# Kernel optimization log

Hardware: AMD Instinct MI355X
Metric: run time of the kernel (lower is better)

Reference implementation:

```python
import jax, jax.numpy as jnp
import numpy as np

N = 50000      # nodes
E = 800000     # edges (avg degree 16)
F_IN = 128     # input feature dim
HID = 64       # hidden_channels
HEADS = 4
OUT = 64       # out_channels


def _gatv2_layer(x, src, dst, Wl, Wr, att, bias, heads, ch, n):
    # lin_l (source) and lin_r (target) projections -> [N, H, C]
    xl = (x @ Wl).reshape(n, heads, ch)
    xr = (x @ Wr).reshape(n, heads, ch)
    # per-edge GATv2 attention logits: a^T LeakyReLU(xl_j + xr_i)
    e = jax.nn.leaky_relu(xl[src] + xr[dst], negative_slope=0.2)  # [E, H, C]
    score = jnp.einsum('ehc,hc->eh', e, att)                      # [E, H]
    # segment softmax over incoming edges of each destination node
    m = jax.ops.segment_max(score, dst, num_segments=n)           # [N, H]
    m = jnp.where(jnp.isfinite(m), m, 0.0)
    p = jnp.exp(score - m[dst])
    denom = jax.ops.segment_sum(p, dst, num_segments=n)           # [N, H]
    alpha = p / (denom[dst] + 1e-16)                              # [E, H]
    # weighted scatter-aggregate of source messages xl_j
    out = jax.ops.segment_sum(alpha[..., None] * xl[src], dst, num_segments=n)
    return out.reshape(n, heads * ch) + bias


def setup_inputs() -> dict:
    key = jax.random.key(0)
    ks = jax.random.split(key, 16)

    def w(k, shape, fan_in):
        return (jax.random.normal(k, shape, dtype=jnp.float32) / np.sqrt(fan_in)).astype(jnp.float32)

    return {
        'x': jax.random.normal(ks[0], (N, F_IN), dtype=jnp.float32),
        'Wl1': w(ks[1], (F_IN, HEADS * HID), F_IN),
        'Wr1': w(ks[2], (F_IN, HEADS * HID), F_IN),
        'att1': w(ks[3], (HEADS, HID), HID),
        'b1': jnp.zeros((HEADS * HID,), jnp.float32),
        'Wl2': w(ks[4], (HEADS * HID, HEADS * HID), HEADS * HID),
        'Wr2': w(ks[5], (HEADS * HID, HEADS * HID), HEADS * HID),
        'att2': w(ks[6], (HEADS, HID), HID),
        'b2': jnp.zeros((HEADS * HID,), jnp.float32),
        'Wl3': w(ks[7], (HEADS * HID, OUT), HEADS * HID),
        'Wr3': w(ks[8], (HEADS * HID, OUT), HEADS * HID),
        'att3': w(ks[9], (1, OUT), OUT),
        'b3': jnp.zeros((OUT,), jnp.float32),
        'Wlin': w(ks[10], (OUT, HID), OUT),
        'blin': jnp.zeros((HID,), jnp.float32),
        'edge_index': jax.random.randint(ks[11], (2, E), 0, N, dtype=jnp.int64
                                         if jax.config.read('jax_enable_x64') else jnp.int32),
    }


def reference(x, Wl1, Wr1, att1, b1, Wl2, Wr2, att2, b2, Wl3, Wr3, att3, b3, Wlin, blin, edge_index):
    src, dst = edge_index[0], edge_index[1]
    h = jax.nn.elu(_gatv2_layer(x, src, dst, Wl1, Wr1, att1, b1, HEADS, HID, N))
    h = jax.nn.elu(_gatv2_layer(h, src, dst, Wl2, Wr2, att2, b2, HEADS, HID, N))
    h = _gatv2_layer(h, src, dst, Wl3, Wr3, att3, b3, 1, OUT, N)
    # F.dropout(p=0.5, training=False) -> identity in eval mode
    return h @ Wlin + blin
```

## Files before the change

kernel.cpp:

```cpp
#include <hip/hip_runtime.h>
#include <hip/hip_fp16.h>

#define NN 50000
#define EE 800000

typedef float f32x4 __attribute__((ext_vector_type(4)));
typedef _Float16 f16x8 __attribute__((ext_vector_type(8)));
typedef _Float16 f16x4 __attribute__((ext_vector_type(4)));
typedef _Float16 f16x2 __attribute__((ext_vector_type(2)));

__global__ void hist_kernel(const int* __restrict__ dst, int* __restrict__ counts, int E) {
    int idx = blockIdx.x * blockDim.x + threadIdx.x;
    int stride = gridDim.x * blockDim.x;
    for (int e = idx; e < E; e += stride)
        atomicAdd(&counts[dst[e]], 1);
}

__global__ void scan_phaseA(const int* __restrict__ counts, int* __restrict__ bsum, int n) {
    __shared__ int buf[256];
    int b = blockIdx.x, t = threadIdx.x;
    int i = b * 256 + t;
    buf[t] = (i < n) ? counts[i] : 0;
    __syncthreads();
#pragma unroll
    for (int off = 128; off; off >>= 1) {
        if (t < off) buf[t] += buf[t + off];
        __syncthreads();
    }
    if (t == 0) bsum[b] = buf[0];
}

__global__ void scan_phaseB(int* __restrict__ bsum, int* __restrict__ row_off_n, int nb) {
    __shared__ int buf[256];
    int t = threadIdx.x;
    int v = (t < nb) ? bsum[t] : 0;
    buf[t] = v;
    __syncthreads();
#pragma unroll
    for (int off = 1; off < 256; off <<= 1) {
        int x = (t >= off) ? buf[t - off] : 0;
        __syncthreads();
        buf[t] += x;
        __syncthreads();
    }
    if (t < nb) bsum[t] = buf[t] - v;
    if (t == 255) *row_off_n = buf[255];
}

__global__ void scan_phaseC(const int* __restrict__ counts, const int* __restrict__ bsum,
                            int* __restrict__ row_off, int n) {
    __shared__ int buf[256];
    int b = blockIdx.x, t = threadIdx.x;
    int i = b * 256 + t;
    int v = (i < n) ? counts[i] : 0;
    buf[t] = v;
    __syncthreads();
#pragma unroll
    for (int off = 1; off < 256; off <<= 1) {
        int x = (t >= off) ? buf[t - off] : 0;
        __syncthreads();
        buf[t] += x;
        __syncthreads();
    }
    if (i < n) row_off[i] = bsum[b] + buf[t] - v;
}

__global__ void scatter_kernel(const int* __restrict__ src, const int* __restrict__ dst,
                               const int* __restrict__ row_off, int* __restrict__ cursor,
                               int* __restrict__ esrc, int E) {
    int idx = blockIdx.x * blockDim.x + threadIdx.x;
    int stride = gridDim.x * blockDim.x;
    for (int e = idx; e < E; e += stride) {
        int d = dst[e];
        int pos = row_off[d] + atomicAdd(&cursor[d], 1);
        esrc[pos] = src[e];
    }
}

__device__ __forceinline__ void wfrag_store(__half* o, int K, int col, int k, float v) {
    int KS = K >> 5;
    int cgni = col >> 4, l15 = col & 15;
    int ks = k >> 5, qq = (k >> 3) & 3, ee = k & 7;
    size_t flat = ((size_t)(cgni * KS + ks) * 64 + qq * 16 + l15) * 8 + ee;
    o[flat] = __float2half_rn(v);
}

__global__ void prep_all(const float* __restrict__ Wl1, const float* __restrict__ Wr1,
                         const float* __restrict__ Wl2, const float* __restrict__ Wr2,
                         const float* __restrict__ Wl3, const float* __restrict__ Wr3,
                         const float* __restrict__ Wlin,
                         __half* __restrict__ w1, __half* __restrict__ w2,
                         __half* __restrict__ w3, __half* __restrict__ w4,
                         const float* __restrict__ x, __half* __restrict__ xf, int n4x) {
    int idx = blockIdx.x * blockDim.x + threadIdx.x;
    if (idx < 233472) {
        const float* W; __half* o; int K, Nc, roff, li;
        if (idx < 65536) {
            K = 128; Nc = 256; o = w1;
            if (idx < 32768) { W = Wl1; li = idx; roff = 0; }
            else             { W = Wr1; li = idx - 32768; roff = 256; }
        } else if (idx < 196608) {
            K = 256; Nc = 256; o = w2;
            if (idx < 131072) { W = Wl2; li = idx - 65536; roff = 0; }
            else              { W = Wr2; li = idx - 131072; roff = 256; }
        } else if (idx < 229376) {
            K = 256; Nc = 64; o = w3;
            if (idx < 212992) { W = Wl3; li = idx - 196608; roff = 0; }
            else              { W = Wr3; li = idx - 212992; roff = 64; }
        } else {
            K = 64; Nc = 64; o = w4; W = Wlin; li = idx - 229376; roff = 0;
        }
        int k = li / Nc, n = li - k * Nc;
        wfrag_store(o, K, roff + n, k, W[li]);
    } else {
        int xi = idx - 233472;
        if (xi < n4x) {
            float4 v = *(const float4*)(x + (size_t)xi * 4);
            f16x4 h = {(_Float16)v.x, (_Float16)v.y, (_Float16)v.z, (_Float16)v.w};
            *(f16x4*)((_Float16*)xf + (size_t)xi * 4) = h;
        }
    }
}

template <int KS, int COLG>
__global__ __launch_bounds__(COLG * 256) void gemm_ws(
        const __half* __restrict__ A, const __half* __restrict__ Bt,
        int M, int nTiles, int Nc, int splitCol,
        __half* __restrict__ outL, __half* __restrict__ outR,
        float* __restrict__ outF, const float* __restrict__ bias) {
    constexpr int K = KS * 32;
    int tid = threadIdx.x;
    int lane = tid & 63;
    int w = tid >> 6;
    int rs = w & 3;
    int cg = w >> 2;
    int l15 = lane & 15, q = lane >> 4;
    int colbase = blockIdx.y * (COLG * 64) + cg * 64;

    const _Float16* Ap = (const _Float16*)A;
    const f16x8* Bf = (const f16x8*)Bt;
    int cgni0 = (blockIdx.y * COLG + cg) * 4;

    f16x8 bfrag[KS][4];
#pragma unroll
    for (int ks = 0; ks < KS; ++ks)
#pragma unroll
        for (int ni = 0; ni < 4; ++ni)
            bfrag[ks][ni] = Bf[((size_t)(cgni0 + ni) * KS + ks) * 64 + lane];

    int tile = blockIdx.x;
    if (tile >= nTiles) return;

    f16x8 afrag[KS];
    {
        int row = tile * 64 + rs * 16 + l15;
        if (row >= M) row = M - 1;
        const _Float16* ap = Ap + (size_t)row * K + q * 8;
#pragma unroll
        for (int ks = 0; ks < KS; ++ks) afrag[ks] = *(const f16x8*)(ap + ks * 32);
    }

    while (true) {
        int next = tile + gridDim.x;
        bool has = (next < nTiles);
        f16x8 anext[KS];
        if (has) {
            int row = next * 64 + rs * 16 + l15;
            if (row >= M) row = M - 1;
            const _Float16* ap = Ap + (size_t)row * K + q * 8;
#pragma unroll
            for (int ks = 0; ks < KS; ++ks) anext[ks] = *(const f16x8*)(ap + ks * 32);
        }

        f32x4 acc[4] = {};
#pragma unroll
        for (int ks = 0; ks < KS; ++ks)
#pragma unroll
            for (int ni = 0; ni < 4; ++ni)
                acc[ni] = __builtin_amdgcn_mfma_f32_16x16x32_f16(afrag[ks], bfrag[ks][ni], acc[ni], 0, 0, 0);

#pragma unroll
        for (int ni = 0; ni < 4; ++ni) {
            int gc = colbase + ni * 16 + l15;
            if (outF) {
                float bv = bias ? bias[gc] : 0.f;
#pragma unroll
                for (int r = 0; r < 4; ++r) {
                    int gr = tile * 64 + rs * 16 + q * 4 + r;
                    if (gr < M) outF[(size_t)gr * Nc + gc] = acc[ni][r] + bv;
                }
            } else {
                __half* dp = outL; int cc = gc;
                if (gc >= splitCol) { dp = outR; cc = gc - splitCol; }
#pragma unroll
                for (int r = 0; r < 4; ++r) {
                    int gr = tile * 64 + rs * 16 + q * 4 + r;
                    if (gr < M) dp[(size_t)gr * splitCol + cc] = __float2half_rn(acc[ni][r]);
                }
            }
        }
        if (!has) break;
#pragma unroll
        for (int ks = 0; ks < KS; ++ks) afrag[ks] = anext[ks];
        tile = next;
    }
}

template <int CTRL>
__device__ __forceinline__ float dpp_add_f32(float x) {
    int y = __builtin_amdgcn_mov_dpp(__float_as_int(x), CTRL, 0xF, 0xF, true);
    return x + __int_as_float(y);
}

__global__ __launch_bounds__(256, 8) void gat_gather_h4(
        const __half* __restrict__ xl, const __half* __restrict__ xr,
        const float* __restrict__ att, const float* __restrict__ bias,
        const int* __restrict__ row_off, const int* __restrict__ esrc,
        __half* __restrict__ out, int n) {
    const float LOG2E = 1.44269504f;
    int wave = threadIdx.x >> 6;
    int lane = threadIdx.x & 63;
    int node = blockIdx.x * 4 + wave;
    if (node >= n) return;
    int slot = lane >> 5;
    unsigned jj = lane & 31;

    const uint4* xl16 = (const uint4*)xl;

    f16x2 xrv[4];
    *(uint4*)(&xrv[0]) = ((const uint4*)xr)[((unsigned)node << 5) + jj];

    float4 a0 = *(const float4*)(att + jj * 8);
    float4 a1 = *(const float4*)(att + jj * 8 + 4);
    f16x2 atv[4] = {
        {(_Float16)(a0.x * LOG2E), (_Float16)(a0.y * LOG2E)},
        {(_Float16)(a0.z * LOG2E), (_Float16)(a0.w * LOG2E)},
        {(_Float16)(a1.x * LOG2E), (_Float16)(a1.y * LOG2E)},
        {(_Float16)(a1.z * LOG2E), (_Float16)(a1.w * LOG2E)}};
    const f16x2 k02 = {(_Float16)0.2f, (_Float16)0.2f};

    float acc[8] = {};
    float L = 0.f;

    int e0 = row_off[node], e1 = row_off[node + 1];
    int elast = (e1 > e0) ? e1 - 1 : 0;

    int sA = esrc[min(e0 + 0 + slot, elast)];
    int sB = esrc[min(e0 + 2 + slot, elast)];
    int sC = esrc[min(e0 + 4 + slot, elast)];
    int sD = esrc[min(e0 + 6 + slot, elast)];
    uint4 A = xl16[((unsigned)sA << 5) + jj];
    uint4 B = xl16[((unsigned)sB << 5) + jj];
    uint4 C = xl16[((unsigned)sC << 5) + jj];
    uint4 D = xl16[((unsigned)sD << 5) + jj];

#define H4_PHASE(BUF, EB)                                                     \
    {                                                                         \
        f16x2 v[4];                                                           \
        *(uint4*)(&v[0]) = BUF;                                               \
        float t = 0.f;                                                        \
        _Pragma("unroll")                                                     \
        for (int k = 0; k < 4; ++k) {                                         \
            f16x2 s = v[k] + xrv[k];                                          \
            f16x2 r = __builtin_elementwise_max(s, s * k02);                  \
            t = __builtin_amdgcn_fdot2(r, atv[k], t, false);                  \
        }                                                                     \
        t = dpp_add_f32<0xB1>(t);                                             \
        t = dpp_add_f32<0x4E>(t);                                             \
        t = dpp_add_f32<0x141>(t);                                            \
        float p = exp2f(t);                                                   \
        p = ((EB) + slot < e1) ? p : 0.f;                                     \
        L += p;                                                               \
        _Pragma("unroll")                                                     \
        for (int k = 0; k < 4; ++k) {                                         \
            acc[2 * k]     = fmaf((float)v[k].x, p, acc[2 * k]);              \
            acc[2 * k + 1] = fmaf((float)v[k].y, p, acc[2 * k + 1]);          \
        }                                                                     \
    }

    {
        int e = e0;
        while (true) {
            int ns = esrc[min(e + 8 + slot, elast)];
            H4_PHASE(A, e)
            A = xl16[((unsigned)ns << 5) + jj];
            e += 2; if (e >= e1) break;
            ns = esrc[min(e + 8 + slot, elast)];
            H4_PHASE(B, e)
            B = xl16[((unsigned)ns << 5) + jj];
            e += 2; if (e >= e1) break;
            ns = esrc[min(e + 8 + slot, elast)];
            H4_PHASE(C, e)
            C = xl16[((unsigned)ns << 5) + jj];
            e += 2; if (e >= e1) break;
            ns = esrc[min(e + 8 + slot, elast)];
            H4_PHASE(D, e)
            D = xl16[((unsigned)ns << 5) + jj];
            e += 2; if (e >= e1) break;
        }
    }
#undef H4_PHASE

#pragma unroll
    for (int k = 0; k < 8; ++k) acc[k] += __shfl_xor(acc[k], 32);
    L += __shfl_xor(L, 32);

    if (slot == 0) {
        float inv = 1.f / (L + 1e-16f);
        float4 b0 = *(const float4*)(bias + jj * 8);
        float4 b1v = *(const float4*)(bias + jj * 8 + 4);
        float bb[8] = {b0.x, b0.y, b0.z, b0.w, b1v.x, b1v.y, b1v.z, b1v.w};
        f16x8 o0;
#pragma unroll
        for (int k = 0; k < 8; ++k) {
            float vA = acc[k] * inv + bb[k];
            vA = vA > 0.f ? vA : __expf(vA) - 1.f;
            o0[k] = (_Float16)vA;
        }
        *(f16x8*)((_Float16*)out + ((size_t)node << 8) + jj * 8) = o0;
    }
}

__global__ __launch_bounds__(256, 8) void gat_gather_h1(
        const __half* __restrict__ xl, const __half* __restrict__ xr,
        const float* __restrict__ att, const float* __restrict__ bias,
        const int* __restrict__ row_off, const int* __restrict__ esrc,
        __half* __restrict__ out, int n) {
    const float LOG2E = 1.44269504f;
    int wave = threadIdx.x >> 6;
    int lane = threadIdx.x & 63;
    int node = blockIdx.x * 4 + wave;
    if (node >= n) return;
    int eslot = lane >> 3;
    unsigned j = lane & 7;

    const uint4* xl16 = (const uint4*)xl;

    f16x2 xrv[4];
    *(uint4*)(&xrv[0]) = ((const uint4*)xr)[((unsigned)node << 3) + j];

    float4 a0 = *(const float4*)(att + j * 8);
    float4 a1 = *(const float4*)(att + j * 8 + 4);
    f16x2 atv[4] = {
        {(_Float16)(a0.x * LOG2E), (_Float16)(a0.y * LOG2E)},
        {(_Float16)(a0.z * LOG2E), (_Float16)(a0.w * LOG2E)},
        {(_Float16)(a1.x * LOG2E), (_Float16)(a1.y * LOG2E)},
        {(_Float16)(a1.z * LOG2E), (_Float16)(a1.w * LOG2E)}};
    const f16x2 k02 = {(_Float16)0.2f, (_Float16)0.2f};

    float acc[8] = {};
    float L = 0.f;

    int e0 = row_off[node], e1 = row_off[node + 1];
    int elast = (e1 > e0) ? e1 - 1 : 0;

    int sA = esrc[min(e0 +  0 + eslot, elast)];
    int sB = esrc[min(e0 +  8 + eslot, elast)];
    int sC = esrc[min(e0 + 16 + eslot, elast)];
    uint4 A = xl16[((unsigned)sA << 3) + j];
    uint4 B = xl16[((unsigned)sB << 3) + j];
    uint4 C = xl16[((unsigned)sC << 3) + j];

#define H1_PHASE(R, EB)                                                       \
    {                                                                         \
        f16x2 v[4];                                                           \
        *(uint4*)(&v[0]) = R;                                                 \
        float t0 = 0.f, t1 = 0.f;                                             \
        {                                                                     \
            f16x2 s0 = v[0] + xrv[0];                                         \
            f16x2 r0 = __builtin_elementwise_max(s0, s0 * k02);               \
            t0 = __builtin_amdgcn_fdot2(r0, atv[0], t0, false);               \
            f16x2 s1 = v[1] + xrv[1];                                         \
            f16x2 r1 = __builtin_elementwise_max(s1, s1 * k02);               \
            t0 = __builtin_amdgcn_fdot2(r1, atv[1], t0, false);               \
            f16x2 s2 = v[2] + xrv[2];                                         \
            f16x2 r2 = __builtin_elementwise_max(s2, s2 * k02);               \
            t1 = __builtin_amdgcn_fdot2(r2, atv[2], t1, false);               \
            f16x2 s3 = v[3] + xrv[3];                                         \
            f16x2 r3 = __builtin_elementwise_max(s3, s3 * k02);               \
            t1 = __builtin_amdgcn_fdot2(r3, atv[3], t1, false);               \
        }                                                                     \
        float t = t0 + t1;                                                    \
        t = dpp_add_f32<0xB1>(t);                                             \
        t = dpp_add_f32<0x4E>(t);                                             \
        t = dpp_add_f32<0x141>(t);                                            \
        float p = exp2f(t);                                                   \
        p = ((EB) + eslot < e1) ? p : 0.f;                                    \
        L += p;                                                               \
        _Pragma("unroll")                                                     \
        for (int k = 0; k < 4; ++k) {                                         \
            acc[2 * k]     = fmaf((float)v[k].x, p, acc[2 * k]);              \
            acc[2 * k + 1] = fmaf((float)v[k].y, p, acc[2 * k + 1]);          \
        }                                                                     \
    }

    {
        int e = e0;
        while (true) {
            int ns = esrc[min(e + 24 + eslot, elast)];
            H1_PHASE(A, e)
            A = xl16[((unsigned)ns << 3) + j];
            e += 8; if (e >= e1) break;
            ns = esrc[min(e + 24 + eslot, elast)];
            H1_PHASE(B, e)
            B = xl16[((unsigned)ns << 3) + j];
            e += 8; if (e >= e1) break;
            ns = esrc[min(e + 24 + eslot, elast)];
            H1_PHASE(C, e)
            C = xl16[((unsigned)ns << 3) + j];
            e += 8; if (e >= e1) break;
        }
    }
#undef H1_PHASE

#pragma unroll
    for (int k = 0; k < 8; ++k) {
        acc[k] += __shfl_xor(acc[k], 8);
        acc[k] += __shfl_xor(acc[k], 16);
        acc[k] += __shfl_xor(acc[k], 32);
    }
    L += __shfl_xor(L, 8);
    L += __shfl_xor(L, 16);
    L += __shfl_xor(L, 32);

    if (eslot == 0) {
        float inv = 1.f / (L + 1e-16f);
        float4 b0 = *(const float4*)(bias + j * 8);
        float4 b1v = *(const float4*)(bias + j * 8 + 4);
        float bb[8] = {b0.x, b0.y, b0.z, b0.w, b1v.x, b1v.y, b1v.z, b1v.w};
        f16x8 ov;
#pragma unroll
        for (int k = 0; k < 8; ++k)
            ov[k] = (_Float16)(acc[k] * inv + bb[k]);
        *(f16x8*)((_Float16*)out + ((size_t)node << 6) + j * 8) = ov;
    }
}

extern "C" void kernel_launch(void* const* d_in, const int* in_sizes, int n_in,
                              void* d_out, int out_size, void* d_ws, size_t ws_size,
                              hipStream_t stream) {
    const float* x    = (const float*)d_in[0];
    const float* Wl1  = (const float*)d_in[1];
    const float* Wr1  = (const float*)d_in[2];
    const float* att1 = (const float*)d_in[3];
    const float* b1   = (const float*)d_in[4];
    const float* Wl2  = (const float*)d_in[5];
    const float* Wr2  = (const float*)d_in[6];
    const float* att2 = (const float*)d_in[7];
    const float* b2   = (const float*)d_in[8];
    const float* Wl3  = (const float*)d_in[9];
    const float* Wr3  = (const float*)d_in[10];
    const float* att3 = (const float*)d_in[11];
    const float* b3   = (const float*)d_in[12];
    const float* Wlin = (const float*)d_in[13];
    const float* blin = (const float*)d_in[14];
    const int*   ei   = (const int*)d_in[15];
    const int* src = ei;
    const int* dst = ei + EE;

    const int N = NN, E = EE;
    const int NB = (N + 255) / 256;

    __half* xf = (__half*)d_ws;
    __half* xl = xf + (size_t)N * 128;
    __half* xr = xl + (size_t)N * 256;
    __half* H  = xr + (size_t)N * 256;
    __half* G  = H + (size_t)N * 256;
    __half* w1 = G + (size_t)N * 64;
    __half* w2 = w1 + 65536;
    __half* w3 = w2 + 131072;
    __half* w4 = w3 + 32768;
    int* row_off = (int*)(w4 + 4096);
    int* tmp     = row_off + (N + 1);
    int* esrc    = tmp + 2 * N;
    int* bsum    = esrc + E;

    hipMemsetAsync(tmp, 0, (size_t)2 * N * sizeof(int), stream);
    hist_kernel<<<1024, 256, 0, stream>>>(dst, tmp, E);
    scan_phaseA<<<NB, 256, 0, stream>>>(tmp, bsum, N);
    scan_phaseB<<<1, 256, 0, stream>>>(bsum, row_off + N, NB);
    scan_phaseC<<<NB, 256, 0, stream>>>(tmp, bsum, row_off, N);
    scatter_kernel<<<1024, 256, 0, stream>>>(src, dst, row_off, tmp + N, esrc, E);

    int n4x = N * 128 / 4;
    prep_all<<<(233472 + n4x + 255) / 256, 256, 0, stream>>>(
        Wl1, Wr1, Wl2, Wr2, Wl3, Wr3, Wlin, w1, w2, w3, w4, x, xf, n4x);

    int nTiles = (N + 63) / 64;
    int gatherBlocks = (N + 3) / 4;

    gemm_ws<4, 2><<<dim3(128, 4), 512, 0, stream>>>(
        xf, w1, N, nTiles, 512, 256, xl, xr, nullptr, nullptr);
    gat_gather_h4<<<gatherBlocks, 256, 0, stream>>>(xl, xr, att1, b1, row_off, esrc, H, N);

    gemm_ws<8, 2><<<dim3(128, 4), 512, 0, stream>>>(
        H, w2, N, nTiles, 512, 256, xl, xr, nullptr, nullptr);
    gat_gather_h4<<<gatherBlocks, 256, 0, stream>>>(xl, xr, att2, b2, row_off, esrc, H, N);

    gemm_ws<8, 2><<<dim3(256, 1), 512, 0, stream>>>(
        H, w3, N, nTiles, 128, 64, xl, xr, nullptr, nullptr);
    gat_gather_h1<<<gatherBlocks, 256, 0, stream>>>(xl, xr, att3, b3, row_off, esrc, G, N);

    gemm_ws<2, 1><<<dim3(512, 1), 256, 0, stream>>>(
        G, w4, N, nTiles, 64, 64, nullptr, nullptr, (float*)d_out, blin);
}
```

Measured before the change: 463.1 us.

## Swizzle GEMM block order, shrink gather blocks, use raw v_exp_f32

Flattens the 2D GEMM grid into a 1D launch and remaps block IDs so that groups of 8 row tiles across all 4 column groups run next to each other. The intent is to improve L2 reuse of the A rows. The gather kernels now run 2 waves per block instead of 4, giving finer scheduling granularity for the irregular per-node edge counts. exp2f is replaced by inline-asm v_exp_f32, which skips the range and denormal handling; this could misbehave on extreme inputs and adds an s_nop.

```diff
diff --git a/kernel.cpp b/kernel.cpp
--- a/kernel.cpp
+++ b/kernel.cpp
@@ -122,7 +122,7 @@
     }
 }
 
-template <int KS, int COLG>
+template <int KS, int COLG, int NBX>
 __global__ __launch_bounds__(COLG * 256) void gemm_ws(
         const __half* __restrict__ A, const __half* __restrict__ Bt,
         int M, int nTiles, int Nc, int splitCol,
@@ -135,11 +135,22 @@
     int rs = w & 3;
     int cg = w >> 2;
     int l15 = lane & 15, q = lane >> 4;
-    int colbase = blockIdx.y * (COLG * 64) + cg * 64;
+
+    int bx, by;
+    if constexpr (NBX > 0) {
+        int bid = blockIdx.x;
+        by = (bid >> 3) & 3;
+        bx = ((bid >> 5) << 3) | (bid & 7);
+    } else {
+        bx = blockIdx.x; by = blockIdx.y;
+    }
+    const int gstride = (NBX > 0) ? NBX : gridDim.x;
+
+    int colbase = by * (COLG * 64) + cg * 64;
 
     const _Float16* Ap = (const _Float16*)A;
     const f16x8* Bf = (const f16x8*)Bt;
-    int cgni0 = (blockIdx.y * COLG + cg) * 4;
+    int cgni0 = (by * COLG + cg) * 4;
 
     f16x8 bfrag[KS][4];
 #pragma unroll
@@ -148,7 +159,7 @@
         for (int ni = 0; ni < 4; ++ni)
             bfrag[ks][ni] = Bf[((size_t)(cgni0 + ni) * KS + ks) * 64 + lane];
 
-    int tile = blockIdx.x;
+    int tile = bx;
     if (tile >= nTiles) return;
 
     f16x8 afrag[KS];
@@ -161,7 +172,7 @@
     }
 
     while (true) {
-        int next = tile + gridDim.x;
+        int next = tile + gstride;
         bool has = (next < nTiles);
         f16x8 anext[KS];
         if (has) {
@@ -212,7 +223,13 @@
     return x + __int_as_float(y);
 }
 
-__global__ __launch_bounds__(256, 8) void gat_gather_h4(
+__device__ __forceinline__ float fast_exp2(float x) {
+    float r;
+    asm("v_exp_f32 %0, %1\n\ts_nop 0" : "=v"(r) : "v"(x));
+    return r;
+}
+
+__global__ __launch_bounds__(128, 8) void gat_gather_h4(
         const __half* __restrict__ xl, const __half* __restrict__ xr,
         const float* __restrict__ att, const float* __restrict__ bias,
         const int* __restrict__ row_off, const int* __restrict__ esrc,
@@ -220,7 +237,7 @@
     const float LOG2E = 1.44269504f;
     int wave = threadIdx.x >> 6;
     int lane = threadIdx.x & 63;
-    int node = blockIdx.x * 4 + wave;
+    int node = blockIdx.x * 2 + wave;
     if (node >= n) return;
     int slot = lane >> 5;
     unsigned jj = lane & 31;
@@ -268,7 +285,7 @@
         t = dpp_add_f32<0xB1>(t);                                             \
         t = dpp_add_f32<0x4E>(t);                                             \
         t = dpp_add_f32<0x141>(t);                                            \
-        float p = exp2f(t);                                                   \
+        float p = fast_exp2(t);                                               \
         p = ((EB) + slot < e1) ? p : 0.f;                                     \
         L += p;                                                               \
         _Pragma("unroll")                                                     \
@@ -321,7 +338,7 @@
     }
 }
 
-__global__ __launch_bounds__(256, 8) void gat_gather_h1(
+__global__ __launch_bounds__(128, 8) void gat_gather_h1(
         const __half* __restrict__ xl, const __half* __restrict__ xr,
         const float* __restrict__ att, const float* __restrict__ bias,
         const int* __restrict__ row_off, const int* __restrict__ esrc,
@@ -329,7 +346,7 @@
     const float LOG2E = 1.44269504f;
     int wave = threadIdx.x >> 6;
     int lane = threadIdx.x & 63;
-    int node = blockIdx.x * 4 + wave;
+    int node = blockIdx.x * 2 + wave;
     if (node >= n) return;
     int eslot = lane >> 3;
     unsigned j = lane & 7;
@@ -384,7 +401,7 @@
         t = dpp_add_f32<0xB1>(t);                                             \
         t = dpp_add_f32<0x4E>(t);                                             \
         t = dpp_add_f32<0x141>(t);                                            \
-        float p = exp2f(t);                                                   \
+        float p = fast_exp2(t);                                               \
         p = ((EB) + eslot < e1) ? p : 0.f;                                    \
         L += p;                                                               \
         _Pragma("unroll")                                                     \
@@ -487,20 +504,20 @@
         Wl1, Wr1, Wl2, Wr2, Wl3, Wr3, Wlin, w1, w2, w3, w4, x, xf, n4x);
 
     int nTiles = (N + 63) / 64;
-    int gatherBlocks = (N + 3) / 4;
-
-    gemm_ws<4, 2><<<dim3(128, 4), 512, 0, stream>>>(
+    int gatherBlocks = (N + 1) / 2;
+
+    gemm_ws<4, 2, 128><<<512, 512, 0, stream>>>(
         xf, w1, N, nTiles, 512, 256, xl, xr, nullptr, nullptr);
-    gat_gather_h4<<<gatherBlocks, 256, 0, stream>>>(xl, xr, att1, b1, row_off, esrc, H, N);
-
-    gemm_ws<8, 2><<<dim3(128, 4), 512, 0, stream>>>(
+    gat_gather_h4<<<gatherBlocks, 128, 0, stream>>>(xl, xr, att1, b1, row_off, esrc, H, N);
+
+    gemm_ws<8, 2, 128><<<512, 512, 0, stream>>>(
         H, w2, N, nTiles, 512, 256, xl, xr, nullptr, nullptr);
-    gat_gather_h4<<<gatherBlocks, 256, 0, stream>>>(xl, xr, att2, b2, row_off, esrc, H, N);
-
-    gemm_ws<8, 2><<<dim3(256, 1), 512, 0, stream>>>(
+    gat_gather_h4<<<gatherBlocks, 128, 0, stream>>>(xl, xr, att2, b2, row_off, esrc, H, N);
+
+    gemm_ws<8, 2, 0><<<dim3(256, 1), 512, 0, stream>>>(
         H, w3, N, nTiles, 128, 64, xl, xr, nullptr, nullptr);
-    gat_gather_h1<<<gatherBlocks, 256, 0, stream>>>(xl, xr, att3, b3, row_off, esrc, G, N);
-
-    gemm_ws<2, 1><<<dim3(512, 1), 256, 0, stream>>>(
+    gat_gather_h1<<<gatherBlocks, 128, 0, stream>>>(xl, xr, att3, b3, row_off, esrc, G, N);
+
+    gemm_ws<2, 1, 0><<<dim3(512, 1), 256, 0, stream>>>(
         G, w4, N, nTiles, 64, 64, nullptr, nullptr, (float*)d_out, blin);
 }
```

After: 457.8 us (median of 2 runs). Within noise of the previous version (-1.1%).
